# Kernel optimization log

Measured on AMD Instinct MI355X. Metric: run time of the kernel, lower is better.

The kernel has to match this reference:

```python
import jax, jax.numpy as jnp
import numpy as np


def setup_inputs() -> dict:
    key = jax.random.key(0)
    kx, kq, kk, kv = jax.random.split(key, 4)
    d_model, d_head = 1024, 64
    x = jax.random.normal(kx, (4, 4096, d_model), dtype=jnp.float32)
    scale = 1.0 / np.sqrt(d_model)
    Wq = jax.random.normal(kq, (d_model, d_head), dtype=jnp.float32) * scale
    Wk = jax.random.normal(kk, (d_model, d_head), dtype=jnp.float32) * scale
    Wv = jax.random.normal(kv, (d_model, d_head), dtype=jnp.float32) * scale
    return {"x": x, "Wq": Wq, "Wk": Wk, "Wv": Wv}


def reference(x, Wq, Wk, Wv):
    # x: [B, S, D]; Wq/Wk/Wv: [D, H]
    d_head = Wq.shape[-1]
    Q = jnp.einsum('bsd,dh->bsh', x, Wq)
    K = jnp.einsum('bsd,dh->bsh', x, Wk)
    V = jnp.einsum('bsd,dh->bsh', x, Wv)
    scores = jnp.einsum('bqh,bkh->bqk', Q, K) / jnp.sqrt(jnp.float32(d_head))
    S = x.shape[1]
    causal = jnp.tril(jnp.ones((S, S), dtype=bool))  # [S, S]
    scores = jnp.where(causal, scores, -jnp.inf)
    weights = jax.nn.softmax(scores, axis=-1)  # [B, S, S]
    return jnp.einsum('bqk,bkh->bqh', weights, V)
```

## Files before the change

### kernel.cpp

```cpp
#include <hip/hip_runtime.h>

#define D_MODEL 1024
#define D_HEAD  64
#define SEQ     4096
#define BATCH   4
#define M_TOT   (BATCH * SEQ)
#define LOG2E   1.44269504088896f
#define MFIX_L2 17.3123404906676f
#define CHUNK   16

typedef __bf16 bf16;
typedef bf16  bf16x8 __attribute__((ext_vector_type(8)));
typedef bf16  bf16x4v __attribute__((ext_vector_type(4)));
typedef float f32x4  __attribute__((ext_vector_type(4)));

#define MFMA(a, b, c) __builtin_amdgcn_mfma_f32_16x16x32_bf16(a, b, c, 0, 0, 0)

#define QKV_OFF  0
#define OBUF_OFF 6291456
#define LBUF_OFF 10485760
#define WT_OFF   10551296
#define VT_OFF   10944512

__global__ void prep_kernel(const float* __restrict__ Wq, const float* __restrict__ Wk,
                            const float* __restrict__ Wv, bf16* __restrict__ Wt,
                            float4* __restrict__ zp, int n4)
{
    const int bx = blockIdx.x;
    const int t  = threadIdx.x;
    if (bx < 48) {
        __shared__ bf16 tr[64][72];
        const int wm = bx >> 4, kt = bx & 15, k0 = kt * 64;
        const float* W = (wm == 0) ? Wq : (wm == 1) ? Wk : Wv;
        const int kr = t >> 2, nb = (t & 3) * 16;
        #pragma unroll
        for (int j = 0; j < 4; j++) {
            float4 wrow = *(const float4*)(W + (size_t)(k0 + kr) * D_HEAD + nb + j * 4);
            tr[nb + j * 4 + 0][kr] = (bf16)wrow.x;
            tr[nb + j * 4 + 1][kr] = (bf16)wrow.y;
            tr[nb + j * 4 + 2][kr] = (bf16)wrow.z;
            tr[nb + j * 4 + 3][kr] = (bf16)wrow.w;
        }
        __syncthreads();
        const int n = t >> 2, kc = (t & 3) * 8;
        bf16* dst = Wt + (size_t)(wm * 64 + n) * D_MODEL + k0;
        #pragma unroll
        for (int h = 0; h < 2; h++) {
            bf16x8 v;
            #pragma unroll
            for (int j = 0; j < 8; j++) v[j] = tr[n][kc + h * 32 + j];
            *(bf16x8*)(dst + kc + h * 32) = v;
        }
    } else {
        int i = (bx - 48) * 256 + t;
        if (i < n4) zp[i] = float4{0.f, 0.f, 0.f, 0.f};
    }
}

#define PXP 40

__global__ __launch_bounds__(256) void proj_kernel(
    const float* __restrict__ x, const bf16* __restrict__ Wt,
    bf16* __restrict__ qkv, bf16* __restrict__ vt)
{
    __shared__ __align__(16) bf16 xs[2][32][PXP];
    __shared__ __align__(16) bf16 ws[2][192][PXP];

    const int t    = threadIdx.x;
    const int nw   = t >> 6;
    const int lane = t & 63;
    const int quad = lane >> 4;
    const int l15  = lane & 15;
    const int row0 = blockIdx.x * 32;

    const int xrow = t >> 3, xk4 = (t & 7) * 4;
    const float* xg = x + (size_t)(row0 + xrow) * D_MODEL + xk4;

    f32x4 acc[6] = {};

    float4 xa;
    bf16x8 wtv[3];

    auto load_regs = [&](int c) {
        xa = *(const float4*)(xg + c * 32);
        #pragma unroll
        for (int it = 0; it < 3; it++) {
            int id = t + it * 256, n = id >> 2, k8 = (id & 3) * 8;
            wtv[it] = *(const bf16x8*)(Wt + (size_t)n * D_MODEL + c * 32 + k8);
        }
    };
    auto store_lds = [&](int p) {
        bf16x4v xv;
        xv[0] = (bf16)xa.x; xv[1] = (bf16)xa.y;
        xv[2] = (bf16)xa.z; xv[3] = (bf16)xa.w;
        *(bf16x4v*)&xs[p][xrow][xk4] = xv;
        #pragma unroll
        for (int it = 0; it < 3; it++) {
            int id = t + it * 256, n = id >> 2, k8 = (id & 3) * 8;
            *(bf16x8*)&ws[p][n][k8] = wtv[it];
        }
    };

    load_regs(0);
    store_lds(0);
    load_regs(1);
    __syncthreads();

    int p = 0;
    for (int c = 0; c < 32; c++) {
        bf16x8 af[2], bfr[3];
        #pragma unroll
        for (int rg = 0; rg < 2; rg++)
            af[rg] = *(bf16x8*)&xs[p][rg * 16 + l15][quad * 8];
        #pragma unroll
        for (int j = 0; j < 3; j++)
            bfr[j] = *(bf16x8*)&ws[p][nw * 48 + j * 16 + l15][quad * 8];
        #pragma unroll
        for (int rg = 0; rg < 2; rg++)
            #pragma unroll
            for (int j = 0; j < 3; j++)
                acc[rg * 3 + j] = MFMA(af[rg], bfr[j], acc[rg * 3 + j]);

        if (c + 1 < 32) {
            store_lds(p ^ 1);
            if (c + 2 < 32) load_regs(c + 2);
        }
        __syncthreads();
        p ^= 1;
    }

    const int bb = row0 >> 12, s0 = row0 & (SEQ - 1);
    #pragma unroll
    for (int rg = 0; rg < 2; rg++)
        #pragma unroll
        for (int j = 0; j < 3; j++) {
            const int col = nw * 48 + j * 16 + l15;
            const int wm = col >> 6, h = col & 63;
            if (wm == 2) {
                bf16x4v vv;
                #pragma unroll
                for (int r = 0; r < 4; r++)
                    vv[r] = (bf16)acc[rg * 3 + j][r];
                *(bf16x4v*)(vt + ((size_t)bb * D_HEAD + h) * SEQ +
                            s0 + rg * 16 + quad * 4) = vv;
            } else {
                const float sc = (wm == 0) ? 0.125f : 1.0f;
                bf16* outp = qkv + (size_t)wm * M_TOT * D_HEAD;
                #pragma unroll
                for (int r = 0; r < 4; r++) {
                    const int row = row0 + rg * 16 + quad * 4 + r;
                    outp[(size_t)row * D_HEAD + h] =
                        (bf16)(acc[rg * 3 + j][r] * sc);
                }
            }
        }
}

__global__ __launch_bounds__(256, 4) void attn_kernel(
    const bf16* __restrict__ qkv, const bf16* __restrict__ vt,
    float* __restrict__ o_buf, float* __restrict__ l_buf)
{
    const int i = blockIdx.x;
    const int c = blockIdx.y;
    const int b = blockIdx.z;
    const int ntiles = i + 1;
    const int tile0  = c * CHUNK;
    if (tile0 >= ntiles) return;
    const int tile1 = min(tile0 + CHUNK, ntiles);

    __shared__ __align__(16) char KsB[2 * 64 * 128];
    __shared__ __align__(16) char VsB[2 * 64 * 128];

    auto kaddr = [](char* base, int pp, int row, int colb) -> void* {
        return base + pp * 8192 + row * 128 + (colb ^ ((row & 7) << 4));
    };

    const bf16* Q = qkv;
    const bf16* K = qkv + (size_t)M_TOT * D_HEAD;

    const int t    = threadIdx.x;
    const int wv   = t >> 6;
    const int lane = t & 63;
    const int quad = lane >> 4;
    const int l15  = lane & 15;
    const int qb   = i * 64;
    const size_t base  = (size_t)b * SEQ * D_HEAD;
    const bf16* vtb = vt + (size_t)b * D_HEAD * SEQ;

    bf16x8 qf0, qf1;
    {
        const bf16* qr = Q + base + (size_t)(qb + wv * 16 + l15) * D_HEAD;
        qf0 = *(const bf16x8*)(qr + quad * 8);
        qf1 = *(const bf16x8*)(qr + 32 + quad * 8);
    }

    f32x4 o[4] = {};
    float lsum = 0.f;
    const int qw0 = qb + wv * 16;

    const int dr  = t >> 2;
    const int cb  = (t & 3) * 16;

    bf16x8 kr0, kr1, vr0, vr1;
    auto load_kv = [&](int tile) {
        const bf16* kp = K + base + (size_t)(tile * 64 + dr) * D_HEAD;
        kr0 = *(const bf16x8*)(kp + (cb >> 1));
        kr1 = *(const bf16x8*)(kp + (cb >> 1) + 32);
        const bf16* vp = vtb + (size_t)dr * SEQ + tile * 64;
        vr0 = *(const bf16x8*)(vp + (cb >> 1));
        vr1 = *(const bf16x8*)(vp + (cb >> 1) + 32);
    };
    auto store_kv = [&](int pp) {
        *(bf16x8*)kaddr(KsB, pp, dr, cb)      = kr0;
        *(bf16x8*)kaddr(KsB, pp, dr, cb + 64) = kr1;
        *(bf16x8*)kaddr(VsB, pp, dr, cb)      = vr0;
        *(bf16x8*)kaddr(VsB, pp, dr, cb + 64) = vr1;
    };

    load_kv(tile0);
    store_kv(0);
    if (tile0 + 1 < tile1) load_kv(tile0 + 1);
    __syncthreads();

    int p = 0;
    for (int tile = tile0; tile < tile1; tile++) {
        const int kk0 = tile * 64;

        f32x4 sc4[4];
        __builtin_amdgcn_s_setprio(1);
        #pragma unroll
        for (int kt = 0; kt < 4; kt++) {
            f32x4 z = {};
            z = MFMA(*(bf16x8*)kaddr(KsB, p, kt * 16 + l15, quad * 16),      qf0, z);
            z = MFMA(*(bf16x8*)kaddr(KsB, p, kt * 16 + l15, 64 + quad * 16), qf1, z);
            sc4[kt] = z;
        }
        __builtin_amdgcn_s_setprio(0);

        bf16 ph[4][4];
        if (tile == i) {
            #pragma unroll
            for (int kt = 0; kt < 4; kt++)
                #pragma unroll
                for (int r = 0; r < 4; r++) {
                    float s = sc4[kt][r];
                    if (kk0 + kt * 16 + quad * 4 + r > qw0 + l15)
                        s = -1e30f;
                    float pe = __builtin_amdgcn_exp2f(fmaf(s, LOG2E, -MFIX_L2));
                    lsum += pe;
                    ph[kt][r] = (bf16)pe;
                }
        } else {
            #pragma unroll
            for (int kt = 0; kt < 4; kt++)
                #pragma unroll
                for (int r = 0; r < 4; r++) {
                    float pe = __builtin_amdgcn_exp2f(
                        fmaf(sc4[kt][r], LOG2E, -MFIX_L2));
                    lsum += pe;
                    ph[kt][r] = (bf16)pe;
                }
        }

        unsigned pku[4][2];
        #pragma unroll
        for (int kt = 0; kt < 4; kt++) {
            __builtin_memcpy(&pku[kt][0], &ph[kt][0], 4);
            __builtin_memcpy(&pku[kt][1], &ph[kt][2], 4);
        }

        const int srcA = l15 + ((lane & 16) ? 32 : 0);
        const int srcB = srcA + 16;
        const bool hi  = (lane & 32) != 0;

        #pragma unroll
        for (int c2 = 0; c2 < 2; c2++) {
            unsigned xA0 = __shfl((int)pku[2 * c2][0],     srcA);
            unsigned xA1 = __shfl((int)pku[2 * c2][1],     srcA);
            unsigned yA0 = __shfl((int)pku[2 * c2 + 1][0], srcA);
            unsigned yA1 = __shfl((int)pku[2 * c2 + 1][1], srcA);
            unsigned xB0 = __shfl((int)pku[2 * c2][0],     srcB);
            unsigned xB1 = __shfl((int)pku[2 * c2][1],     srcB);
            unsigned yB0 = __shfl((int)pku[2 * c2 + 1][0], srcB);
            unsigned yB1 = __shfl((int)pku[2 * c2 + 1][1], srcB);
            unsigned fr[4];
            fr[0] = hi ? yA0 : xA0;
            fr[1] = hi ? yA1 : xA1;
            fr[2] = hi ? yB0 : xB0;
            fr[3] = hi ? yB1 : xB1;
            bf16x8 pa;
            __builtin_memcpy(&pa, fr, 16);

            __builtin_amdgcn_s_setprio(1);
            #pragma unroll
            for (int t4 = 0; t4 < 4; t4++) {
                bf16x8 vb = *(bf16x8*)kaddr(VsB, p, t4 * 16 + l15,
                                            c2 * 64 + quad * 16);
                o[t4] = MFMA(pa, vb, o[t4]);
            }
            __builtin_amdgcn_s_setprio(0);
        }

        if (tile + 1 < tile1) {
            store_kv(p ^ 1);
            if (tile + 2 < tile1) load_kv(tile + 2);
            __syncthreads();
        }
        p ^= 1;
    }

    const int mrow0 = b * SEQ + qw0;
    lsum += __shfl_xor(lsum, 16, 64);
    lsum += __shfl_xor(lsum, 32, 64);
    if (lane < 16)
        atomicAdd(&l_buf[mrow0 + l15], lsum);
    #pragma unroll
    for (int r = 0; r < 4; r++) {
        const size_t orow = (size_t)(mrow0 + quad * 4 + r) * D_HEAD;
        #pragma unroll
        for (int t4 = 0; t4 < 4; t4++)
            atomicAdd(&o_buf[orow + t4 * 16 + l15], o[t4][r]);
    }
}

__global__ void norm_kernel(const float4* __restrict__ o_buf,
                            const float* __restrict__ l_buf,
                            float4* __restrict__ out)
{
    int gid = blockIdx.x * 256 + threadIdx.x;
    int m = gid >> 4;
    float inv = 1.0f / l_buf[m];
    float4 v = o_buf[gid];
    out[gid] = float4{v.x * inv, v.y * inv, v.z * inv, v.w * inv};
}

extern "C" void kernel_launch(void* const* d_in, const int* in_sizes, int n_in,
                              void* d_out, int out_size, void* d_ws, size_t ws_size,
                              hipStream_t stream) {
    const float* x  = (const float*)d_in[0];
    const float* Wq = (const float*)d_in[1];
    const float* Wk = (const float*)d_in[2];
    const float* Wv = (const float*)d_in[3];

    bf16*  qkv   = (bf16*)((char*)d_ws + QKV_OFF);
    float* o_buf = (float*)((char*)d_ws + OBUF_OFF);
    float* l_buf = (float*)((char*)d_ws + LBUF_OFF);
    bf16*  Wt    = (bf16*)((char*)d_ws + WT_OFF);
    bf16*  vt    = (bf16*)((char*)d_ws + VT_OFF);

    const int zero4 = (M_TOT * 65) / 4;
    const int zblocks = (zero4 + 255) / 256;
    prep_kernel<<<48 + zblocks, 256, 0, stream>>>(Wq, Wk, Wv, Wt,
                                                  (float4*)o_buf, zero4);
    proj_kernel<<<M_TOT / 32, 256, 0, stream>>>(x, Wt, qkv, vt);
    attn_kernel<<<dim3(SEQ / 64, SEQ / 64 / CHUNK, BATCH), 256, 0, stream>>>(
        qkv, vt, o_buf, l_buf);
    norm_kernel<<<M_TOT * 16 / 256, 256, 0, stream>>>((const float4*)o_buf, l_buf,
                                                      (float4*)d_out);
}
```

Before: 159.0 us.

## Deepen QKV projection prefetch to two stages and use LDS-only barriers

The QKV projection loop now keeps two register sets of global loads in flight (A/B ping-pong), unrolled by two, so each global load has a full extra iteration to land before its LDS store. Both kernels replace __syncthreads with a barrier that waits only on lgkmcnt, so outstanding global loads (vmcnt) are not drained at each barrier. This targets global memory latency stalls at barriers. The cost is higher register pressure from the doubled prefetch buffers, which may reduce occupancy.

```diff
diff --git a/kernel.cpp b/kernel.cpp
--- a/kernel.cpp
+++ b/kernel.cpp
@@ -15,6 +15,13 @@
 typedef float f32x4  __attribute__((ext_vector_type(4)));
 
 #define MFMA(a, b, c) __builtin_amdgcn_mfma_f32_16x16x32_bf16(a, b, c, 0, 0, 0)
+
+__device__ __forceinline__ void barrier_release_lds() {
+    __builtin_amdgcn_sched_barrier(0);
+    asm volatile("s_waitcnt lgkmcnt(0)" ::: "memory");
+    __builtin_amdgcn_s_barrier();
+    __builtin_amdgcn_sched_barrier(0);
+}
 
 #define QKV_OFF  0
 #define OBUF_OFF 6291456
@@ -78,36 +85,48 @@
 
     f32x4 acc[6] = {};
 
-    float4 xa;
-    bf16x8 wtv[3];
-
-    auto load_regs = [&](int c) {
-        xa = *(const float4*)(xg + c * 32);
+    float4 xaA, xaB;
+    bf16x8 wtvA[3], wtvB[3];
+
+    auto loadA = [&](int c) {
+        xaA = *(const float4*)(xg + c * 32);
         #pragma unroll
         for (int it = 0; it < 3; it++) {
             int id = t + it * 256, n = id >> 2, k8 = (id & 3) * 8;
-            wtv[it] = *(const bf16x8*)(Wt + (size_t)n * D_MODEL + c * 32 + k8);
-        }
-    };
-    auto store_lds = [&](int p) {
-        bf16x4v xv;
-        xv[0] = (bf16)xa.x; xv[1] = (bf16)xa.y;
-        xv[2] = (bf16)xa.z; xv[3] = (bf16)xa.w;
-        *(bf16x4v*)&xs[p][xrow][xk4] = xv;
+            wtvA[it] = *(const bf16x8*)(Wt + (size_t)n * D_MODEL + c * 32 + k8);
+        }
+    };
+    auto loadB = [&](int c) {
+        xaB = *(const float4*)(xg + c * 32);
         #pragma unroll
         for (int it = 0; it < 3; it++) {
             int id = t + it * 256, n = id >> 2, k8 = (id & 3) * 8;
-            *(bf16x8*)&ws[p][n][k8] = wtv[it];
-        }
-    };
-
-    load_regs(0);
-    store_lds(0);
-    load_regs(1);
-    __syncthreads();
-
-    int p = 0;
-    for (int c = 0; c < 32; c++) {
+            wtvB[it] = *(const bf16x8*)(Wt + (size_t)n * D_MODEL + c * 32 + k8);
+        }
+    };
+    auto storeA = [&](int p) {
+        bf16x4v xv;
+        xv[0] = (bf16)xaA.x; xv[1] = (bf16)xaA.y;
+        xv[2] = (bf16)xaA.z; xv[3] = (bf16)xaA.w;
+        *(bf16x4v*)&xs[p][xrow][xk4] = xv;
+        #pragma unroll
+        for (int it = 0; it < 3; it++) {
+            int id = t + it * 256, n = id >> 2, k8 = (id & 3) * 8;
+            *(bf16x8*)&ws[p][n][k8] = wtvA[it];
+        }
+    };
+    auto storeB = [&](int p) {
+        bf16x4v xv;
+        xv[0] = (bf16)xaB.x; xv[1] = (bf16)xaB.y;
+        xv[2] = (bf16)xaB.z; xv[3] = (bf16)xaB.w;
+        *(bf16x4v*)&xs[p][xrow][xk4] = xv;
+        #pragma unroll
+        for (int it = 0; it < 3; it++) {
+            int id = t + it * 256, n = id >> 2, k8 = (id & 3) * 8;
+            *(bf16x8*)&ws[p][n][k8] = wtvB[it];
+        }
+    };
+    auto compute = [&](int p) {
         bf16x8 af[2], bfr[3];
         #pragma unroll
         for (int rg = 0; rg < 2; rg++)
@@ -120,12 +139,25 @@
             #pragma unroll
             for (int j = 0; j < 3; j++)
                 acc[rg * 3 + j] = MFMA(af[rg], bfr[j], acc[rg * 3 + j]);
-
-        if (c + 1 < 32) {
-            store_lds(p ^ 1);
-            if (c + 2 < 32) load_regs(c + 2);
-        }
-        __syncthreads();
+    };
+
+    loadA(0);
+    storeA(0);
+    loadB(1);
+    loadA(2);
+    barrier_release_lds();
+
+    int p = 0;
+    for (int c = 0; c < 32; c += 2) {
+        compute(p);
+        storeB(p ^ 1);
+        if (c + 3 < 32) loadB(c + 3);
+        barrier_release_lds();
+        p ^= 1;
+        compute(p);
+        if (c + 2 < 32) storeA(p ^ 1);
+        if (c + 4 < 32) loadA(c + 4);
+        barrier_release_lds();
         p ^= 1;
     }
 
@@ -220,7 +252,7 @@
     load_kv(tile0);
     store_kv(0);
     if (tile0 + 1 < tile1) load_kv(tile0 + 1);
-    __syncthreads();
+    barrier_release_lds();
 
     int p = 0;
     for (int tile = tile0; tile < tile1; tile++) {
@@ -304,7 +336,7 @@
         if (tile + 1 < tile1) {
             store_kv(p ^ 1);
             if (tile + 2 < tile1) load_kv(tile + 2);
-            __syncthreads();
+            barrier_release_lds();
         }
         p ^= 1;
     }
```

New measurement: 157.5 us. Within noise of the previous version (-1.0%).

## Stage projection tiles via direct global-to-LDS loads with swizzled layout

Applied to the files above, without the earlier changes.

The projection kernel now copies raw fp32 x and bf16 weight tiles straight into LDS with global_load_lds, instead of going through registers. It uses XOR-swizzled rows, a K chunk of 64 with double buffering, and converts x to bf16 when fragments are read. It also adds a launch bounds hint for two blocks per CU. In the attention kernel, __syncthreads is replaced by a custom barrier that waits only on LDS counters, so outstanding global prefetches stay in flight. This removes the register round trip and the VGPR pressure, at the cost of more LDS traffic from reading fp32 A data and converting it repeatedly.

```diff
diff --git a/kernel.cpp b/kernel.cpp
--- a/kernel.cpp
+++ b/kernel.cpp
@@ -15,6 +15,26 @@
 typedef float f32x4  __attribute__((ext_vector_type(4)));
 
 #define MFMA(a, b, c) __builtin_amdgcn_mfma_f32_16x16x32_bf16(a, b, c, 0, 0, 0)
+
+__device__ __forceinline__ void barrier_release_lds() {
+    __builtin_amdgcn_sched_barrier(0);
+    asm volatile("s_waitcnt lgkmcnt(0)" ::: "memory");
+    __builtin_amdgcn_s_barrier();
+    __builtin_amdgcn_sched_barrier(0);
+}
+
+__device__ __forceinline__ void phase_barrier() {
+    __builtin_amdgcn_sched_barrier(0);
+    asm volatile("s_waitcnt vmcnt(0)" ::: "memory");
+    __builtin_amdgcn_s_barrier();
+    __builtin_amdgcn_sched_barrier(0);
+}
+
+__device__ __forceinline__ void gld16(const void* g, void* l) {
+    __builtin_amdgcn_global_load_lds(
+        (const __attribute__((address_space(1))) void*)g,
+        (__attribute__((address_space(3))) void*)l, 16, 0, 0);
+}
 
 #define QKV_OFF  0
 #define OBUF_OFF 6291456
@@ -57,76 +77,92 @@
     }
 }
 
-#define PXP 40
-
-__global__ __launch_bounds__(256) void proj_kernel(
+__global__ __launch_bounds__(256, 2) void proj_kernel(
     const float* __restrict__ x, const bf16* __restrict__ Wt,
     bf16* __restrict__ qkv, bf16* __restrict__ vt)
 {
-    __shared__ __align__(16) bf16 xs[2][32][PXP];
-    __shared__ __align__(16) bf16 ws[2][192][PXP];
+    __shared__ __align__(16) char Al[2][32 * 256];
+    __shared__ __align__(16) char Bl[2][192 * 128];
 
     const int t    = threadIdx.x;
-    const int nw   = t >> 6;
+    const int wv   = t >> 6;
     const int lane = t & 63;
     const int quad = lane >> 4;
     const int l15  = lane & 15;
     const int row0 = blockIdx.x * 32;
 
-    const int xrow = t >> 3, xk4 = (t & 7) * 4;
-    const float* xg = x + (size_t)(row0 + xrow) * D_MODEL + xk4;
+    const char* xb = (const char*)x;
+    const char* wb = (const char*)Wt;
 
     f32x4 acc[6] = {};
 
-    float4 xa;
-    bf16x8 wtv[3];
-
-    auto load_regs = [&](int c) {
-        xa = *(const float4*)(xg + c * 32);
-        #pragma unroll
-        for (int it = 0; it < 3; it++) {
-            int id = t + it * 256, n = id >> 2, k8 = (id & 3) * 8;
-            wtv[it] = *(const bf16x8*)(Wt + (size_t)n * D_MODEL + c * 32 + k8);
-        }
-    };
-    auto store_lds = [&](int p) {
-        bf16x4v xv;
-        xv[0] = (bf16)xa.x; xv[1] = (bf16)xa.y;
-        xv[2] = (bf16)xa.z; xv[3] = (bf16)xa.w;
-        *(bf16x4v*)&xs[p][xrow][xk4] = xv;
-        #pragma unroll
-        for (int it = 0; it < 3; it++) {
-            int id = t + it * 256, n = id >> 2, k8 = (id & 3) * 8;
-            *(bf16x8*)&ws[p][n][k8] = wtv[it];
-        }
-    };
-
-    load_regs(0);
-    store_lds(0);
-    load_regs(1);
-    __syncthreads();
-
-    int p = 0;
-    for (int c = 0; c < 32; c++) {
-        bf16x8 af[2], bfr[3];
-        #pragma unroll
-        for (int rg = 0; rg < 2; rg++)
-            af[rg] = *(bf16x8*)&xs[p][rg * 16 + l15][quad * 8];
-        #pragma unroll
-        for (int j = 0; j < 3; j++)
-            bfr[j] = *(bf16x8*)&ws[p][nw * 48 + j * 16 + l15][quad * 8];
-        #pragma unroll
-        for (int rg = 0; rg < 2; rg++)
-            #pragma unroll
-            for (int j = 0; j < 3; j++)
-                acc[rg * 3 + j] = MFMA(af[rg], bfr[j], acc[rg * 3 + j]);
-
-        if (c + 1 < 32) {
-            store_lds(p ^ 1);
-            if (c + 2 < 32) load_regs(c + 2);
-        }
-        __syncthreads();
-        p ^= 1;
+    auto stageA = [&](int bsel, int step) {
+        #pragma unroll
+        for (int i = 0; i < 2; i++) {
+            const int s  = wv * 2 + i;
+            const int r  = s * 4 + (lane >> 4);
+            const int cs = ((lane & 15) * 16) ^ ((r & 7) << 4);
+            const void* g = xb + (size_t)(row0 + r) * 4096 + step * 256 + cs;
+            gld16(g, (char*)Al[bsel] + s * 1024);
+        }
+    };
+    auto stageB = [&](int bsel, int step) {
+        #pragma unroll
+        for (int i = 0; i < 6; i++) {
+            const int s  = wv * 6 + i;
+            const int n  = s * 8 + (lane >> 3);
+            const int cs = ((lane & 7) * 16) ^ ((n & 7) << 4);
+            const void* g = wb + (size_t)n * 2048 + step * 128 + cs;
+            gld16(g, (char*)Bl[bsel] + s * 1024);
+        }
+    };
+
+    auto cvt8 = [](float4 lo, float4 hi) {
+        bf16x8 r;
+        r[0] = (bf16)lo.x; r[1] = (bf16)lo.y; r[2] = (bf16)lo.z; r[3] = (bf16)lo.w;
+        r[4] = (bf16)hi.x; r[5] = (bf16)hi.y; r[6] = (bf16)hi.z; r[7] = (bf16)hi.w;
+        return r;
+    };
+
+    auto compute = [&](int bsel) {
+        const char* Ab = Al[bsel];
+        const char* Bb = Bl[bsel];
+        #pragma unroll
+        for (int ks = 0; ks < 2; ks++) {
+            bf16x8 afr[2];
+            #pragma unroll
+            for (int rg = 0; rg < 2; rg++) {
+                const int r  = rg * 16 + l15;
+                const int o  = ks * 128 + quad * 32;
+                const int m  = (r & 7) << 4;
+                float4 lo = *(const float4*)(Ab + r * 256 + (o ^ m));
+                float4 hi = *(const float4*)(Ab + r * 256 + ((o + 16) ^ m));
+                afr[rg] = cvt8(lo, hi);
+            }
+            #pragma unroll
+            for (int j = 0; j < 3; j++) {
+                const int n  = wv * 48 + j * 16 + l15;
+                const int o  = ks * 64 + quad * 16;
+                bf16x8 bfrg = *(const bf16x8*)(Bb + n * 128 + (o ^ ((n & 7) << 4)));
+                acc[0 * 3 + j] = MFMA(afr[0], bfrg, acc[0 * 3 + j]);
+                acc[1 * 3 + j] = MFMA(afr[1], bfrg, acc[1 * 3 + j]);
+            }
+        }
+    };
+
+    stageA(0, 0);
+    stageB(0, 0);
+    phase_barrier();
+
+    int buf = 0;
+    for (int s = 0; s < 16; s++) {
+        if (s + 1 < 16) {
+            stageA(buf ^ 1, s + 1);
+            stageB(buf ^ 1, s + 1);
+        }
+        compute(buf);
+        phase_barrier();
+        buf ^= 1;
     }
 
     const int bb = row0 >> 12, s0 = row0 & (SEQ - 1);
@@ -134,7 +170,7 @@
     for (int rg = 0; rg < 2; rg++)
         #pragma unroll
         for (int j = 0; j < 3; j++) {
-            const int col = nw * 48 + j * 16 + l15;
+            const int col = wv * 48 + j * 16 + l15;
             const int wm = col >> 6, h = col & 63;
             if (wm == 2) {
                 bf16x4v vv;
@@ -220,7 +256,7 @@
     load_kv(tile0);
     store_kv(0);
     if (tile0 + 1 < tile1) load_kv(tile0 + 1);
-    __syncthreads();
+    barrier_release_lds();
 
     int p = 0;
     for (int tile = tile0; tile < tile1; tile++) {
@@ -304,7 +340,7 @@
         if (tile + 1 < tile1) {
             store_kv(p ^ 1);
             if (tile + 2 < tile1) load_kv(tile + 2);
-            __syncthreads();
+            barrier_release_lds();
         }
         p ^= 1;
     }
```

Result: faster. 149.1 us (-6.2%).
